# Performance work log

Measured on AMD Instinct MI355X. Metric: run time of the kernel, lower is better.

The kernel has to match this reference:

```python
import jax, jax.numpy as jnp
import numpy as np

NHO, NFO = 400000, 100000
EHO, EFO, EBI = 4000000, 2000000, 800000
NUM_CLASSES = 10


def _gcn_conv(x, W, b, src, dst, w, n):
    # PyG GCNConv with edge weights + default self-loops (weight 1):
    # deg[i] = sum_{e: dst(e)=i} w_e + 1 ; norm_e = d^{-1/2}[src] * w_e * d^{-1/2}[dst]
    deg = jax.ops.segment_sum(w, dst, num_segments=n) + 1.0
    dinv = jax.lax.rsqrt(deg)
    xw = x @ W                                    # [n, out]
    coef = dinv[src] * w * dinv[dst]              # [E]
    agg = jax.ops.segment_sum(xw[src] * coef[:, None], dst, num_segments=n)
    # self-loop contribution: dinv[i]*1*dinv[i] = 1/deg[i]
    return agg + xw * (dinv * dinv)[:, None] + b


def setup_inputs() -> dict:
    key = jax.random.key(0)
    ks = jax.random.split(key, 24)
    def lin(i, fin, fout, s=None):
        s = 1.0 / np.sqrt(fin) if s is None else s
        return jax.random.uniform(ks[i], (fin, fout), jnp.float32, -s, s)
    inp = {
        'x_ho': jax.random.normal(ks[0], (NHO, 60), jnp.float32),
        'x_fo': jax.random.normal(ks[1], (NFO, 32), jnp.float32),
        'ho_src': jax.random.randint(ks[2], (EHO,), 0, NHO, jnp.int32),
        'ho_dst': jax.random.randint(ks[3], (EHO,), 0, NHO, jnp.int32),
        'ho_w': jax.random.uniform(ks[4], (EHO,), jnp.float32),
        'fo_src': jax.random.randint(ks[5], (EFO,), 0, NFO, jnp.int32),
        'fo_dst': jax.random.randint(ks[6], (EFO,), 0, NFO, jnp.int32),
        'fo_w': jax.random.uniform(ks[7], (EFO,), jnp.float32),
        'bi_src': jax.random.randint(ks[8], (EBI,), 0, NHO, jnp.int32),
        'bi_dst': jax.random.randint(ks[9], (EBI,), 0, NFO, jnp.int32),
        'num_ho_nodes': NHO,
        'num_fo_nodes': NFO,
        # GCNConv params (weight [in,out], bias [out])
        'W220': lin(10, 60, 16), 'b220': jnp.zeros((16,), jnp.float32),
        'W221': lin(11, 16, 32), 'b221': jnp.zeros((32,), jnp.float32),
        'W110': lin(12, 32, 16), 'b110': jnp.zeros((16,), jnp.float32),
        'W111': lin(13, 16, 32), 'b111': jnp.zeros((32,), jnp.float32),
        # BipartiteGraphOperator linears
        'lin1_w': lin(14, 32, 32), 'lin1_b': jax.random.uniform(ks[15], (32,), jnp.float32, -0.17, 0.17),
        'lin2_w': lin(16, 32, 32), 'lin2_b': jax.random.uniform(ks[17], (32,), jnp.float32, -0.17, 0.17),
        # output MLP
        'mlp_w': lin(18, 32, NUM_CLASSES), 'mlp_b': jnp.zeros((NUM_CLASSES,), jnp.float32),
    }
    return inp


def reference(x_ho, x_fo, ho_src, ho_dst, ho_w, fo_src, fo_dst, fo_w,
              bi_src, bi_dst, num_ho_nodes, num_fo_nodes,
              W220, b220, W221, b221, W110, b110, W111, b111,
              lin1_w, lin1_b, lin2_w, lin2_b, mlp_w, mlp_b):
    elu = jax.nn.elu
    # dropout is identity in eval mode
    # HO branch (GCN stack on higher-order graph)
    h = elu(_gcn_conv(x_ho, W220, b220, ho_src, ho_dst, ho_w, num_ho_nodes))
    h = elu(_gcn_conv(h, W221, b221, ho_src, ho_dst, ho_w, num_ho_nodes))
    # FO branch (GCN stack on first-order graph)
    h1 = elu(_gcn_conv(x_fo, W110, b110, fo_src, fo_dst, fo_w, num_fo_nodes))
    h1 = elu(_gcn_conv(h1, W111, b111, fo_src, fo_dst, fo_w, num_fo_nodes))
    # Bipartite operator: default MessagePassing message is x_j (source side),
    # aggregated 'add' at targets; lin2(h1) is computed but unused by default semantics.
    m = h @ lin1_w + lin1_b                              # [NHO, 32]
    _unused = h1 @ lin2_w + lin2_b                       # faithful to original (dead value)
    agg = jax.ops.segment_sum(m[bi_src], bi_dst, num_segments=num_fo_nodes)  # [NFO, 32]
    out = elu(agg)
    return out @ mlp_w + mlp_b                           # [NFO, num_classes]
```

## Files before the change

### kernel.cpp

```cpp
#include <hip/hip_runtime.h>
#include <hip/hip_fp16.h>
#include <math.h>

#define SCAN_BLOCK 1024
#define BK_BITS 9
#define BKSZ 512
#define CH 16384
#define FXS 33554432.0f

static __device__ __forceinline__ float elu_f(float x) {
    return x > 0.0f ? x : expm1f(x);
}


__global__ __launch_bounds__(256) void k_passA(
    const int* __restrict__ hd, int* __restrict__ counts, int nChunks, int Eho, int NB,
    const int* __restrict__ bd, int* __restrict__ cntBI, unsigned short* __restrict__ rankBI,
    int Ebi, int biB,
    const float* __restrict__ x, const float* __restrict__ W, __half* __restrict__ Axw, int N)
{
    __shared__ float smem[64 * 61 + 960];
    int bid = blockIdx.x;
    if (bid < nChunks) {
        unsigned* h = (unsigned*)smem;
        for (int t = threadIdx.x; t < NB; t += 256) h[t] = 0u;
        __syncthreads();
        int e0 = bid * CH;
        int e1 = e0 + CH; if (e1 > Eho) e1 = Eho;
        for (int e = e0 + threadIdx.x; e < e1; e += 256)
            atomicAdd(&h[(unsigned)hd[e] >> BK_BITS], 1u);
        __syncthreads();
        for (int t = threadIdx.x; t < NB; t += 256)
            counts[(size_t)t * nChunks + bid] = (int)h[t];
        return;
    }
    bid -= nChunks;
    if (bid < biB) {
        int i = bid * 256 + threadIdx.x;
        int stride = biB * 256;
        for (; i < Ebi; i += stride)
            rankBI[i] = (unsigned short)atomicAdd(&cntBI[bd[i]], 1);
        return;
    }
    bid -= biB;
    float* sx = smem;
    float* sW = smem + 64 * 61;
    for (int t = threadIdx.x; t < 960; t += 256) sW[t] = W[t];
    int base = bid * 64;
    int rows = N - base; if (rows > 64) rows = 64;
    const float4* xg = (const float4*)(x + (size_t)base * 60);
    int nf4 = rows * 15;
    for (int j = threadIdx.x; j < nf4; j += 256) {
        float4 v = xg[j];
        int r = j / 15, k4 = j - r * 15;
        float* dst = &sx[r * 61 + k4 * 4];
        dst[0] = v.x; dst[1] = v.y; dst[2] = v.z; dst[3] = v.w;
    }
    __syncthreads();
    int t = threadIdx.x;
    if (t < rows) {
        const float* xr = &sx[t * 61];
        float acc[16];
        #pragma unroll
        for (int o = 0; o < 16; o++) acc[o] = 0.0f;
        #pragma unroll
        for (int k = 0; k < 60; k++) {
            float xv = xr[k];
            #pragma unroll
            for (int o = 0; o < 16; o++) acc[o] = fmaf(xv, sW[k * 16 + o], acc[o]);
        }
        __half2 hh[8];
        #pragma unroll
        for (int j = 0; j < 8; j++) hh[j] = __floats2half2_rn(acc[2 * j], acc[2 * j + 1]);
        uint4* yr = (uint4*)(Axw + (size_t)(base + t) * 16);
        yr[0] = *(uint4*)&hh[0];
        yr[1] = *(uint4*)&hh[4];
    }
}


__global__ void k_scan2(const int* __restrict__ in1, int* __restrict__ out1, int n1, int nb1,
                        const int* __restrict__ in2, int* __restrict__ out2, int n2,
                        int* __restrict__ sums1, int* __restrict__ sums2) {
    __shared__ int tmp[SCAN_BLOCK];
    int b = blockIdx.x;
    const int* in; int* out; int n; int* sums; int bb;
    if (b < nb1) { in = in1; out = out1; n = n1; sums = sums1; bb = b; }
    else         { in = in2; out = out2; n = n2; sums = sums2; bb = b - nb1; }
    int gid = bb * SCAN_BLOCK + threadIdx.x;
    int v = (gid < n) ? in[gid] : 0;
    tmp[threadIdx.x] = v;
    __syncthreads();
    for (int off = 1; off < SCAN_BLOCK; off <<= 1) {
        int t = (threadIdx.x >= off) ? tmp[threadIdx.x - off] : 0;
        __syncthreads();
        tmp[threadIdx.x] += t;
        __syncthreads();
    }
    if (gid < n) out[gid] = tmp[threadIdx.x] - v;
    if (threadIdx.x == SCAN_BLOCK - 1) sums[bb] = tmp[threadIdx.x];
}

__global__ void k_scan_sums2(int* __restrict__ sums1, int nb1,
                             int* __restrict__ sums2, int nb2) {
    __shared__ int tmp[SCAN_BLOCK];
    int* s = (blockIdx.x == 0) ? sums1 : sums2;
    int nb = (blockIdx.x == 0) ? nb1 : nb2;
    int v = (threadIdx.x < nb) ? s[threadIdx.x] : 0;
    tmp[threadIdx.x] = v;
    __syncthreads();
    for (int off = 1; off < SCAN_BLOCK; off <<= 1) {
        int t = (threadIdx.x >= off) ? tmp[threadIdx.x - off] : 0;
        __syncthreads();
        tmp[threadIdx.x] += t;
        __syncthreads();
    }
    if (threadIdx.x < nb) s[threadIdx.x] = tmp[threadIdx.x] - v;
}

__global__ void k_scan_add2(int* __restrict__ out1, const int* __restrict__ sums1,
                            int n1, int tot1, int nb1,
                            int* __restrict__ out2, const int* __restrict__ sums2,
                            int n2, int tot2) {
    int b = blockIdx.x;
    if (b < nb1) {
        int gid = b * SCAN_BLOCK + threadIdx.x;
        if (gid < n1) out1[gid] += sums1[b];
        if (gid == 0) out1[n1] = tot1;
    } else {
        int b2 = b - nb1;
        int gid = b2 * SCAN_BLOCK + threadIdx.x;
        if (gid < n2) out2[gid] += sums2[b2];
        if (gid == 0) out2[n2] = tot2;
    }
}


__global__ __launch_bounds__(256) void k_passC(
    const int* __restrict__ hs, const int* __restrict__ hd, const float* __restrict__ hw,
    const int* __restrict__ countsS, int nChunks, int NB, int Eho,
    int2* __restrict__ eS,
    const int* __restrict__ bs, const int* __restrict__ bd,
    const unsigned short* __restrict__ rankBI, const int* __restrict__ rsbi,
    int* __restrict__ srcbi, int Ebi)
{
    __shared__ int cur[1024];
    int bid = blockIdx.x;
    if (bid < nChunks) {
        for (int t = threadIdx.x; t < NB; t += 256)
            cur[t] = countsS[(size_t)t * nChunks + bid];
        __syncthreads();
        int e0 = bid * CH;
        int e1 = e0 + CH; if (e1 > Eho) e1 = Eho;
        for (int e = e0 + threadIdx.x; e < e1; e += 256) {
            int d = hd[e];
            int pos = atomicAdd(&cur[(unsigned)d >> BK_BITS], 1);
            eS[pos] = make_int2(hs[e] | ((d & (BKSZ - 1)) << 19), __float_as_int(hw[e]));
        }
        return;
    }
    bid -= nChunks;
    int i = bid * 256 + threadIdx.x;
    int stride = ((int)gridDim.x - nChunks) * 256;
    for (; i < Ebi; i += stride)
        srcbi[rsbi[bd[i]] + rankBI[i]] = bs[i];
}


__global__ __launch_bounds__(1024) void k_passD(
    const int2* __restrict__ eS, const int* __restrict__ countsS, int nChunks,
    int NB, int Eho, int NHO,
    int2* __restrict__ pairs, int* __restrict__ rs_ho, float* __restrict__ dinv,
    __half* __restrict__ Ah)
{
    __shared__ unsigned cnt[BKSZ];
    __shared__ unsigned fx[BKSZ];
    __shared__ int sc[BKSZ];
    __shared__ int cur[BKSZ];
    __shared__ float sdinv[BKSZ];
    int b = blockIdx.x;
    int base = countsS[(size_t)b * nChunks];
    int end  = (b == NB - 1) ? Eho : countsS[(size_t)(b + 1) * nChunks];
    int tid = threadIdx.x;
    if (tid < BKSZ) { cnt[tid] = 0u; fx[tid] = 0u; }
    __syncthreads();
    for (int e = base + tid; e < end; e += 1024) {
        int2 p = eS[e];
        int n = (unsigned)p.x >> 19;
        atomicAdd(&cnt[n], 1u);
        atomicAdd(&fx[n], (unsigned)(__int_as_float(p.y) * FXS + 0.5f));
    }
    __syncthreads();
    if (tid < BKSZ) sc[tid] = (int)cnt[tid];
    __syncthreads();
    for (int off = 1; off < BKSZ; off <<= 1) {
        int t = (tid < BKSZ && tid >= off) ? sc[tid - off] : 0;
        __syncthreads();
        if (tid < BKSZ) sc[tid] += t;
        __syncthreads();
    }
    int gbase = b * BKSZ;
    int nn = NHO - gbase; if (nn > BKSZ) nn = BKSZ;
    if (tid < BKSZ) {
        int gn = gbase + tid;
        if (gn < NHO) {
            int off0 = sc[tid] - (int)cnt[tid];
            cur[tid] = base + off0;
            rs_ho[gn] = base + off0;
            float di = rsqrtf((float)fx[tid] * (1.0f / FXS) + 1.0f);
            dinv[gn] = di;
            sdinv[tid] = di;
        }
    }
    if (b == NB - 1 && tid == 0) rs_ho[NHO] = Eho;
    __syncthreads();
    for (int e = base + tid; e < end; e += 1024) {
        int2 p = eS[e];
        int n = (unsigned)p.x >> 19;
        int pos = atomicAdd(&cur[n], 1);
        pairs[pos] = make_int2(p.x & 0x7FFFF, p.y);
    }
    for (int idx = tid; idx < nn * 16; idx += 1024) {
        int n = idx >> 4;
        size_t a = (size_t)(gbase + n) * 16 + (idx & 15);
        Ah[a] = __float2half_rn(__half2float(Ah[a]) * sdinv[n]);
    }
}

#define EDGE_FMA(TAB, J) \
    acc = fmaf(__int_as_float(__shfl(p.y, (J), 16)), \
               __half2float(TAB[(size_t)__shfl(p.x, (J), 16) * 16 + ln]), acc);


__global__ void k_gather1(const int2* __restrict__ pairs, const int* __restrict__ rs,
                          const float* __restrict__ dinv, const __half* __restrict__ A,
                          const float* __restrict__ b, __half* __restrict__ B, int N) {
    int t = blockIdx.x * blockDim.x + threadIdx.x;
    int node = t >> 4, ln = t & 15;
    if (node >= N) return;
    int beg = rs[node], end = rs[node + 1];
    float acc = 0.0f;
    for (int k = beg; k < end; k += 16) {
        int take = end - k; if (take > 16) take = 16;
        int2 p = pairs[k + (ln < take ? ln : take - 1)];
        if (take == 16) {
            #pragma unroll
            for (int j = 0; j < 16; j++) { EDGE_FMA(A, j) }
        } else {
            int j = 0;
            if (take >= 8) {
                #pragma unroll
                for (int jj = 0; jj < 8; jj++) { EDGE_FMA(A, jj) }
                j = 8;
            }
            if (take - j >= 4) {
                #pragma unroll
                for (int jj = 0; jj < 4; jj++) { EDGE_FMA(A, j + jj) }
                j += 4;
            }
            for (; j < take; j++) { EDGE_FMA(A, j) }
        }
    }
    float di = dinv[node];
    float v = fmaf(di, acc + __half2float(A[(size_t)node * 16 + ln]), b[ln]);
    B[(size_t)node * 16 + ln] = __float2half_rn(di * elu_f(v));
}


__global__ void k_gather2(const int2* __restrict__ pairs, const int* __restrict__ rs,
                          const float* __restrict__ dinv, const __half* __restrict__ B,
                          const float* __restrict__ W221, const float* __restrict__ b221,
                          const float* __restrict__ L1w, const float* __restrict__ L1b,
                          __half* __restrict__ M, int N) {
    __shared__ float sW[16 * 32];
    __shared__ float sb2[32];
    __shared__ float sL[32 * 32];
    __shared__ float sLb[32];
    for (int t = threadIdx.x; t < 512; t += blockDim.x) sW[t] = W221[t];
    for (int t = threadIdx.x; t < 1024; t += blockDim.x) sL[t] = L1w[t];
    if (threadIdx.x < 32) { sb2[threadIdx.x] = b221[threadIdx.x]; sLb[threadIdx.x] = L1b[threadIdx.x]; }
    __syncthreads();
    int t = blockIdx.x * blockDim.x + threadIdx.x;
    int node = t >> 4, ln = t & 15;
    if (node >= N) return;
    int beg = rs[node], end = rs[node + 1];
    float acc = 0.0f;
    for (int k = beg; k < end; k += 16) {
        int take = end - k; if (take > 16) take = 16;
        int2 p = pairs[k + (ln < take ? ln : take - 1)];
        if (take == 16) {
            #pragma unroll
            for (int j = 0; j < 16; j++) { EDGE_FMA(B, j) }
        } else {
            int j = 0;
            if (take >= 8) {
                #pragma unroll
                for (int jj = 0; jj < 8; jj++) { EDGE_FMA(B, jj) }
                j = 8;
            }
            if (take - j >= 4) {
                #pragma unroll
                for (int jj = 0; jj < 4; jj++) { EDGE_FMA(B, j + jj) }
                j += 4;
            }
            for (; j < take; j++) { EDGE_FMA(B, j) }
        }
    }
    float di = dinv[node];
    float agg = di * (acc + __half2float(B[(size_t)node * 16 + ln]));
    float h2a = sb2[ln], h2b = sb2[ln + 16];
    #pragma unroll
    for (int k = 0; k < 16; k++) {
        float ak = __shfl(agg, k, 16);
        h2a += ak * sW[k * 32 + ln];
        h2b += ak * sW[k * 32 + ln + 16];
    }
    h2a = elu_f(h2a); h2b = elu_f(h2b);
    float m0 = sLb[ln], m1 = sLb[ln + 16];
    #pragma unroll
    for (int k = 0; k < 16; k++) {
        float a0 = __shfl(h2a, k, 16);
        float a1 = __shfl(h2b, k, 16);
        m0 += a0 * sL[k * 32 + ln]        + a1 * sL[(k + 16) * 32 + ln];
        m1 += a0 * sL[k * 32 + ln + 16]   + a1 * sL[(k + 16) * 32 + ln + 16];
    }
    __half* mr = M + (size_t)node * 32;
    mr[ln] = __float2half_rn(m0); mr[ln + 16] = __float2half_rn(m1);
}


__global__ void k_bi_mlp(const int* __restrict__ srcs, const int* __restrict__ rs,
                         const __half* __restrict__ M, const float* __restrict__ mw,
                         const float* __restrict__ mb, float* __restrict__ out, int N) {
    __shared__ float sW[32 * 10];
    __shared__ float sb[10];
    for (int t = threadIdx.x; t < 320; t += blockDim.x) sW[t] = mw[t];
    if (threadIdx.x < 10) sb[threadIdx.x] = mb[threadIdx.x];
    __syncthreads();
    int t = blockIdx.x * blockDim.x + threadIdx.x;
    int node = t >> 5, ln = t & 31;
    if (node >= N) return;
    int beg = rs[node], end = rs[node + 1];
    float acc = 0.0f;
    for (int k = beg; k < end; k += 32) {
        int take = end - k; if (take > 32) take = 32;
        int ms = srcs[k + (ln < take ? ln : take - 1)];
        if (take == 32) {
            #pragma unroll
            for (int j = 0; j < 32; j++)
                acc += __half2float(M[(size_t)__shfl(ms, j, 32) * 32 + ln]);
        } else {
            int j = 0;
            if (take >= 16) {
                #pragma unroll
                for (int jj = 0; jj < 16; jj++)
                    acc += __half2float(M[(size_t)__shfl(ms, jj, 32) * 32 + ln]);
                j = 16;
            }
            if (take - j >= 8) {
                #pragma unroll
                for (int jj = 0; jj < 8; jj++)
                    acc += __half2float(M[(size_t)__shfl(ms, j + jj, 32) * 32 + ln]);
                j += 8;
            }
            if (take - j >= 4) {
                #pragma unroll
                for (int jj = 0; jj < 4; jj++)
                    acc += __half2float(M[(size_t)__shfl(ms, j + jj, 32) * 32 + ln]);
                j += 4;
            }
            for (; j < take; j++)
                acc += __half2float(M[(size_t)__shfl(ms, j, 32) * 32 + ln]);
        }
    }
    float e = elu_f(acc);
    int lw = ln < 10 ? ln : 0;
    float o = ln < 10 ? sb[ln] : 0.0f;
    #pragma unroll
    for (int k = 0; k < 32; k++) {
        float ak = __shfl(e, k, 32);
        o += ak * sW[k * 10 + lw];
    }
    if (ln < 10) out[(size_t)node * 10 + ln] = o;
}


extern "C" void kernel_launch(void* const* d_in, const int* in_sizes, int n_in,
                              void* d_out, int out_size, void* d_ws, size_t ws_size,
                              hipStream_t stream) {
    const float* x_ho   = (const float*)d_in[0];
    const int*   ho_src = (const int*)d_in[2];
    const int*   ho_dst = (const int*)d_in[3];
    const float* ho_w   = (const float*)d_in[4];
    const int*   bi_src = (const int*)d_in[8];
    const int*   bi_dst = (const int*)d_in[9];
    const float* W220   = (const float*)d_in[12];
    const float* b220   = (const float*)d_in[13];
    const float* W221   = (const float*)d_in[14];
    const float* b221   = (const float*)d_in[15];
    const float* lin1_w = (const float*)d_in[20];
    const float* lin1_b = (const float*)d_in[21];
    const float* mlp_w  = (const float*)d_in[24];
    const float* mlp_b  = (const float*)d_in[25];

    const int NHO = in_sizes[0] / 60;
    const int EHO = in_sizes[2];
    const int EBI = in_sizes[8];
    const int NFO = out_size / 10;
    float* out = (float*)d_out;

    const int NB = (NHO + BKSZ - 1) / BKSZ;
    const int nChunks = (EHO + CH - 1) / CH;
    const int NC = NB * nChunks;
    const int biB = 2048;
    const int xwB = (NHO + 63) / 64;

    size_t off = 0;
    float* ws = (float*)d_ws;
    int2*  pairs = (int2*)(ws + off); off += (size_t)2 * EHO;
    size_t uWords = (size_t)2 * EHO;
    if ((size_t)8 * NHO > uWords) uWords = (size_t)8 * NHO;
    int2*   eS = (int2*)(ws + off);
    __half* B  = (__half*)(ws + off); off += uWords;
    __half* A  = (__half*)(ws + off); off += (size_t)16 * NHO;
    __half* M  = A;
    float* dinv  = ws + off; off += NHO;
    int*   rs_ho = (int*)(ws + off); off += NHO + 1;
    int*   counts  = (int*)(ws + off); off += NC;
    int*   countsS = (int*)(ws + off); off += NC + 1;
    int*   cntBI = (int*)(ws + off); off += NFO;
    int*   rs_bi = (int*)(ws + off); off += NFO + 1;
    int*   srcbi = (int*)(ws + off); off += EBI;
    unsigned short* rankBI = (unsigned short*)(ws + off); off += (EBI + 1) / 2;
    int*   sums1 = (int*)(ws + off); off += SCAN_BLOCK;
    int*   sums2 = (int*)(ws + off); off += SCAN_BLOCK;

    const int BLK = 256;
    const int nb1 = (NC + SCAN_BLOCK - 1) / SCAN_BLOCK;
    const int nb2 = (NFO + SCAN_BLOCK - 1) / SCAN_BLOCK;

    hipMemsetAsync(cntBI, 0, (size_t)NFO * 4, stream);

    k_passA<<<nChunks + biB + xwB, BLK, 0, stream>>>(
        ho_dst, counts, nChunks, EHO, NB,
        bi_dst, cntBI, rankBI, EBI, biB,
        x_ho, W220, A, NHO);

    k_scan2<<<nb1 + nb2, SCAN_BLOCK, 0, stream>>>(
        counts, countsS, NC, nb1, cntBI, rs_bi, NFO, sums1, sums2);
    k_scan_sums2<<<2, SCAN_BLOCK, 0, stream>>>(sums1, nb1, sums2, nb2);
    k_scan_add2<<<nb1 + nb2, SCAN_BLOCK, 0, stream>>>(
        countsS, sums1, NC, EHO, nb1, rs_bi, sums2, NFO, EBI);

    k_passC<<<nChunks + 2048, BLK, 0, stream>>>(
        ho_src, ho_dst, ho_w, countsS, nChunks, NB, EHO, eS,
        bi_src, bi_dst, rankBI, rs_bi, srcbi, EBI);

    k_passD<<<NB, SCAN_BLOCK, 0, stream>>>(
        eS, countsS, nChunks, NB, EHO, NHO, pairs, rs_ho, dinv, A);

    {
        long long t = (long long)NHO * 16;
        k_gather1<<<(int)((t + BLK - 1) / BLK), BLK, 0, stream>>>(
            pairs, rs_ho, dinv, A, b220, B, NHO);
    }
    {
        long long t = (long long)NHO * 16;
        k_gather2<<<(int)((t + BLK - 1) / BLK), BLK, 0, stream>>>(
            pairs, rs_ho, dinv, B, W221, b221, lin1_w, lin1_b, M, NHO);
    }
    {
        long long t = (long long)NFO * 32;
        k_bi_mlp<<<(int)((t + BLK - 1) / BLK), BLK, 0, stream>>>(
            srcbi, rs_bi, M, mlp_w, mlp_b, out, NFO);
    }
}
```

Before: 457.2 us.

## Gather half2 feature pairs with 8 lanes per node, stage aggregates in LDS

The two HO-graph gather kernels now give each node 8 lanes instead of 16, with each lane loading a __half2 (two features), so every edge needs half as many lanes and shuffles. k_gather2 is split into two phases: a gather phase of 32 nodes per 256-thread block that writes aggregated features to shared memory, then a 16-lanes-per-node phase for the dense 16x32 and 32x32 transforms. The aim is to cut per-edge shuffle and instruction overhead and improve occupancy on the memory-bound gathers, at the cost of an extra block barrier and a shared-memory round trip. The rs_ho workspace buffer is also moved later in the layout.

```diff
diff --git a/kernel.cpp b/kernel.cpp
--- a/kernel.cpp
+++ b/kernel.cpp
@@ -227,105 +227,111 @@
     }
 }
 
-#define EDGE_FMA(TAB, J) \
-    acc = fmaf(__int_as_float(__shfl(p.y, (J), 16)), \
-               __half2float(TAB[(size_t)__shfl(p.x, (J), 16) * 16 + ln]), acc);
+#define EDGE_FMA2(TAB2, J) { \
+    int px_ = __shfl(p.x, (J), 8); \
+    float w_ = __int_as_float(__shfl(p.y, (J), 8)); \
+    float2 v_ = __half22float2(TAB2[(size_t)px_ * 8 + ln]); \
+    ax = fmaf(w_, v_.x, ax); ay = fmaf(w_, v_.y, ay); }
+
+#define EDGE_LOOP2(TAB2) \
+    for (int k = beg; k < end; k += 8) { \
+        int take = end - k; if (take > 8) take = 8; \
+        int2 p = pairs[k + (ln < take ? ln : take - 1)]; \
+        if (take == 8) { \
+            _Pragma("unroll") \
+            for (int j = 0; j < 8; j++) { EDGE_FMA2(TAB2, j) } \
+        } else { \
+            int j = 0; \
+            if (take >= 4) { \
+                _Pragma("unroll") \
+                for (int jj = 0; jj < 4; jj++) { EDGE_FMA2(TAB2, jj) } \
+                j = 4; \
+            } \
+            if (take - j >= 2) { \
+                EDGE_FMA2(TAB2, j) EDGE_FMA2(TAB2, j + 1) \
+                j += 2; \
+            } \
+            if (j < take) { EDGE_FMA2(TAB2, j) } \
+        } \
+    }
 
 
 __global__ void k_gather1(const int2* __restrict__ pairs, const int* __restrict__ rs,
-                          const float* __restrict__ dinv, const __half* __restrict__ A,
-                          const float* __restrict__ b, __half* __restrict__ B, int N) {
+                          const float* __restrict__ dinv, const __half2* __restrict__ A2,
+                          const float* __restrict__ b, __half2* __restrict__ B2, int N) {
     int t = blockIdx.x * blockDim.x + threadIdx.x;
-    int node = t >> 4, ln = t & 15;
+    int node = t >> 3, ln = t & 7;
     if (node >= N) return;
     int beg = rs[node], end = rs[node + 1];
-    float acc = 0.0f;
-    for (int k = beg; k < end; k += 16) {
-        int take = end - k; if (take > 16) take = 16;
-        int2 p = pairs[k + (ln < take ? ln : take - 1)];
-        if (take == 16) {
-            #pragma unroll
-            for (int j = 0; j < 16; j++) { EDGE_FMA(A, j) }
-        } else {
-            int j = 0;
-            if (take >= 8) {
-                #pragma unroll
-                for (int jj = 0; jj < 8; jj++) { EDGE_FMA(A, jj) }
-                j = 8;
-            }
-            if (take - j >= 4) {
-                #pragma unroll
-                for (int jj = 0; jj < 4; jj++) { EDGE_FMA(A, j + jj) }
-                j += 4;
-            }
-            for (; j < take; j++) { EDGE_FMA(A, j) }
-        }
-    }
+    float ax = 0.0f, ay = 0.0f;
+    EDGE_LOOP2(A2)
     float di = dinv[node];
-    float v = fmaf(di, acc + __half2float(A[(size_t)node * 16 + ln]), b[ln]);
-    B[(size_t)node * 16 + ln] = __float2half_rn(di * elu_f(v));
-}
-
-
-__global__ void k_gather2(const int2* __restrict__ pairs, const int* __restrict__ rs,
-                          const float* __restrict__ dinv, const __half* __restrict__ B,
-                          const float* __restrict__ W221, const float* __restrict__ b221,
-                          const float* __restrict__ L1w, const float* __restrict__ L1b,
-                          __half* __restrict__ M, int N) {
+    float2 sl = __half22float2(A2[(size_t)node * 8 + ln]);
+    float vx = fmaf(di, ax + sl.x, b[2 * ln]);
+    float vy = fmaf(di, ay + sl.y, b[2 * ln + 1]);
+    B2[(size_t)node * 8 + ln] = __floats2half2_rn(di * elu_f(vx), di * elu_f(vy));
+}
+
+
+__global__ __launch_bounds__(256) void k_gather2(
+    const int2* __restrict__ pairs, const int* __restrict__ rs,
+    const float* __restrict__ dinv, const __half2* __restrict__ B2,
+    const float* __restrict__ W221, const float* __restrict__ b221,
+    const float* __restrict__ L1w, const float* __restrict__ L1b,
+    __half* __restrict__ M, int N)
+{
     __shared__ float sW[16 * 32];
     __shared__ float sb2[32];
     __shared__ float sL[32 * 32];
     __shared__ float sLb[32];
-    for (int t = threadIdx.x; t < 512; t += blockDim.x) sW[t] = W221[t];
-    for (int t = threadIdx.x; t < 1024; t += blockDim.x) sL[t] = L1w[t];
-    if (threadIdx.x < 32) { sb2[threadIdx.x] = b221[threadIdx.x]; sLb[threadIdx.x] = L1b[threadIdx.x]; }
-    __syncthreads();
-    int t = blockIdx.x * blockDim.x + threadIdx.x;
-    int node = t >> 4, ln = t & 15;
-    if (node >= N) return;
-    int beg = rs[node], end = rs[node + 1];
-    float acc = 0.0f;
-    for (int k = beg; k < end; k += 16) {
-        int take = end - k; if (take > 16) take = 16;
-        int2 p = pairs[k + (ln < take ? ln : take - 1)];
-        if (take == 16) {
+    __shared__ float sAgg[32][17];
+    int tid = threadIdx.x;
+    for (int t = tid; t < 512; t += 256) sW[t] = W221[t];
+    for (int t = tid; t < 1024; t += 256) sL[t] = L1w[t];
+    if (tid < 32) { sb2[tid] = b221[tid]; sLb[tid] = L1b[tid]; }
+    __syncthreads();
+
+    int nodeBase = blockIdx.x * 32;
+    {
+        int n8 = tid >> 3, ln = tid & 7;
+        int node = nodeBase + n8;
+        if (node < N) {
+            int beg = rs[node], end = rs[node + 1];
+            float ax = 0.0f, ay = 0.0f;
+            EDGE_LOOP2(B2)
+            float di = dinv[node];
+            float2 sl = __half22float2(B2[(size_t)node * 8 + ln]);
+            sAgg[n8][2 * ln]     = di * (ax + sl.x);
+            sAgg[n8][2 * ln + 1] = di * (ay + sl.y);
+        }
+    }
+    __syncthreads();
+    int n16 = tid >> 4, l16 = tid & 15;
+    #pragma unroll
+    for (int it = 0; it < 2; ++it) {
+        int n = it * 16 + n16;
+        int gn = nodeBase + n;
+        if (gn < N) {
+            float h2a = sb2[l16], h2b = sb2[l16 + 16];
             #pragma unroll
-            for (int j = 0; j < 16; j++) { EDGE_FMA(B, j) }
-        } else {
-            int j = 0;
-            if (take >= 8) {
-                #pragma unroll
-                for (int jj = 0; jj < 8; jj++) { EDGE_FMA(B, jj) }
-                j = 8;
+            for (int k = 0; k < 16; k++) {
+                float ak = sAgg[n][k];
+                h2a += ak * sW[k * 32 + l16];
+                h2b += ak * sW[k * 32 + l16 + 16];
             }
-            if (take - j >= 4) {
-                #pragma unroll
-                for (int jj = 0; jj < 4; jj++) { EDGE_FMA(B, j + jj) }
-                j += 4;
+            h2a = elu_f(h2a); h2b = elu_f(h2b);
+            float m0 = sLb[l16], m1 = sLb[l16 + 16];
+            #pragma unroll
+            for (int k = 0; k < 16; k++) {
+                float a0 = __shfl(h2a, k, 16);
+                float a1 = __shfl(h2b, k, 16);
+                m0 += a0 * sL[k * 32 + l16]        + a1 * sL[(k + 16) * 32 + l16];
+                m1 += a0 * sL[k * 32 + l16 + 16]   + a1 * sL[(k + 16) * 32 + l16 + 16];
             }
-            for (; j < take; j++) { EDGE_FMA(B, j) }
-        }
-    }
-    float di = dinv[node];
-    float agg = di * (acc + __half2float(B[(size_t)node * 16 + ln]));
-    float h2a = sb2[ln], h2b = sb2[ln + 16];
-    #pragma unroll
-    for (int k = 0; k < 16; k++) {
-        float ak = __shfl(agg, k, 16);
-        h2a += ak * sW[k * 32 + ln];
-        h2b += ak * sW[k * 32 + ln + 16];
-    }
-    h2a = elu_f(h2a); h2b = elu_f(h2b);
-    float m0 = sLb[ln], m1 = sLb[ln + 16];
-    #pragma unroll
-    for (int k = 0; k < 16; k++) {
-        float a0 = __shfl(h2a, k, 16);
-        float a1 = __shfl(h2b, k, 16);
-        m0 += a0 * sL[k * 32 + ln]        + a1 * sL[(k + 16) * 32 + ln];
-        m1 += a0 * sL[k * 32 + ln + 16]   + a1 * sL[(k + 16) * 32 + ln + 16];
-    }
-    __half* mr = M + (size_t)node * 32;
-    mr[ln] = __float2half_rn(m0); mr[ln + 16] = __float2half_rn(m1);
+            __half* mr = M + (size_t)gn * 32;
+            mr[l16] = __float2half_rn(m0); mr[l16 + 16] = __float2half_rn(m1);
+        }
+    }
 }
 
 
@@ -425,12 +431,12 @@
     __half* A  = (__half*)(ws + off); off += (size_t)16 * NHO;
     __half* M  = A;
     float* dinv  = ws + off; off += NHO;
-    int*   rs_ho = (int*)(ws + off); off += NHO + 1;
     int*   counts  = (int*)(ws + off); off += NC;
     int*   countsS = (int*)(ws + off); off += NC + 1;
     int*   cntBI = (int*)(ws + off); off += NFO;
     int*   rs_bi = (int*)(ws + off); off += NFO + 1;
     int*   srcbi = (int*)(ws + off); off += EBI;
+    int*   rs_ho = (int*)(ws + off); off += NHO + 1;
     unsigned short* rankBI = (unsigned short*)(ws + off); off += (EBI + 1) / 2;
     int*   sums1 = (int*)(ws + off); off += SCAN_BLOCK;
     int*   sums2 = (int*)(ws + off); off += SCAN_BLOCK;
@@ -460,14 +466,14 @@
         eS, countsS, nChunks, NB, EHO, NHO, pairs, rs_ho, dinv, A);
 
     {
-        long long t = (long long)NHO * 16;
+        long long t = (long long)NHO * 8;
         k_gather1<<<(int)((t + BLK - 1) / BLK), BLK, 0, stream>>>(
-            pairs, rs_ho, dinv, A, b220, B, NHO);
+            pairs, rs_ho, dinv, (const __half2*)A, b220, (__half2*)B, NHO);
     }
     {
-        long long t = (long long)NHO * 16;
-        k_gather2<<<(int)((t + BLK - 1) / BLK), BLK, 0, stream>>>(
-            pairs, rs_ho, dinv, B, W221, b221, lin1_w, lin1_b, M, NHO);
+        int g = (NHO + 31) / 32;
+        k_gather2<<<g, BLK, 0, stream>>>(
+            pairs, rs_ho, dinv, (const __half2*)B, W221, b221, lin1_w, lin1_b, M, NHO);
     }
     {
         long long t = (long long)NFO * 32;
```

New measurement: 436.4 us. 1.05x faster.
